# Performance work log

Hardware: AMD Instinct MI355X
Metric: run time of the kernel (lower is better)

The kernel has to match this reference:

```python
import jax, jax.numpy as jnp
import numpy as np

N_NODES = 50000
HIDDEN = 128
IN_DIM = 128
N_EDGES = 1600000


def gcn_conv(x, W, b, src, dst, deg_isqrt, n_nodes):
    # x: [N, Fin], W: [Fin, Fout]. src/dst include self-loops.
    h = x @ W  # [N, Fout]
    norm = deg_isqrt[src] * deg_isqrt[dst]  # [E+N]
    msgs = h[src] * norm[:, None]  # [E+N, Fout]
    agg = jax.ops.segment_sum(msgs, dst, num_segments=n_nodes)
    return agg + b


def setup_inputs() -> dict:
    key = jax.random.key(0)
    ks = jax.random.split(key, 8)
    x = jax.random.normal(ks[0], (N_NODES, IN_DIM), dtype=jnp.float32)
    edge_index = jax.random.randint(ks[1], (2, N_EDGES), 0, N_NODES, dtype=jnp.int64 if jax.config.jax_enable_x64 else jnp.int32)
    s1 = 1.0 / np.sqrt(IN_DIM)
    s2 = 1.0 / np.sqrt(HIDDEN)
    W1 = jax.random.uniform(ks[2], (IN_DIM, HIDDEN), jnp.float32, -s1, s1)
    b1 = jnp.zeros((HIDDEN,), jnp.float32)
    W2 = jax.random.uniform(ks[3], (HIDDEN, HIDDEN), jnp.float32, -s2, s2)
    b2 = jnp.zeros((HIDDEN,), jnp.float32)
    Wc = jax.random.uniform(ks[4], (HIDDEN, 1), jnp.float32, -s2, s2)
    bc = jnp.zeros((1,), jnp.float32)
    return {"x": x, "edge_index": edge_index, "W1": W1, "b1": b1,
            "W2": W2, "b2": b2, "Wc": Wc, "bc": bc}


def reference(x, edge_index, W1, b1, W2, b2, Wc, bc):
    n = x.shape[0]
    # add self-loops (PyG GCNConv default)
    loop = jnp.arange(n, dtype=edge_index.dtype)
    src = jnp.concatenate([edge_index[0], loop])
    dst = jnp.concatenate([edge_index[1], loop])
    # symmetric normalization: deg over augmented dst, edge weight 1
    deg = jax.ops.segment_sum(jnp.ones_like(dst, dtype=x.dtype), dst, num_segments=n)
    deg_isqrt = jnp.where(deg > 0, jax.lax.rsqrt(deg), 0.0)
    h = jax.nn.relu(gcn_conv(x, W1, b1, src, dst, deg_isqrt, n))
    h = jax.nn.relu(gcn_conv(h, W2, b2, src, dst, deg_isqrt, n))
    return (h @ Wc + bc).squeeze(-1)  # [N]
```

## Files before the change

### kernel.cpp

```cpp
#include <hip/hip_runtime.h>
#include <hip/hip_fp16.h>
#include <cstdint>


#define EPBH 4096
#define DCAP 9216

__global__ __launch_bounds__(256) void bucket_hist(const int* __restrict__ dst,
                                                   int* __restrict__ hist,
                                                   int ne, int nb, int nbuck) {
  __shared__ int lh[256];
  lh[threadIdx.x] = 0;
  __syncthreads();
  int base = blockIdx.x * EPBH;
#pragma unroll
  for (int j = 0; j < 16; ++j) {
    int e = base + j * 256 + threadIdx.x;
    if (e < ne) {
      int d = __builtin_nontemporal_load(&dst[e]);
      atomicAdd(&lh[d >> 8], 1);
    }
  }
  __syncthreads();
  if (threadIdx.x < nbuck)
    hist[(size_t)threadIdx.x * nb + blockIdx.x] = lh[threadIdx.x];
}

__global__ void scan_block(const int* __restrict__ in, int* __restrict__ part,
                           int* __restrict__ bsum, int n) {
  __shared__ int s[1024];
  int i = blockIdx.x * 1024 + threadIdx.x;
  int v = (i < n) ? in[i] : 0;
  s[threadIdx.x] = v;
  __syncthreads();
  for (int off = 1; off < 1024; off <<= 1) {
    int t = (threadIdx.x >= (unsigned)off) ? s[threadIdx.x - off] : 0;
    __syncthreads();
    s[threadIdx.x] += t;
    __syncthreads();
  }
  if (i < n) part[i] = s[threadIdx.x] - v;
  if (threadIdx.x == 1023) bsum[blockIdx.x] = s[1023];
}

__global__ void scan_partials(int* __restrict__ bsum, int nb) {
  __shared__ int s[256];
  int v = (threadIdx.x < (unsigned)nb) ? bsum[threadIdx.x] : 0;
  s[threadIdx.x] = v;
  __syncthreads();
  for (int off = 1; off < 256; off <<= 1) {
    int t = (threadIdx.x >= (unsigned)off) ? s[threadIdx.x - off] : 0;
    __syncthreads();
    s[threadIdx.x] += t;
    __syncthreads();
  }
  if (threadIdx.x < (unsigned)nb) bsum[threadIdx.x] = s[threadIdx.x] - v;
}

__global__ void finalize_scan(const int* __restrict__ part, const int* __restrict__ bsum,
                              int* __restrict__ out, int n) {
  int i = blockIdx.x * blockDim.x + threadIdx.x;
  if (i < n) out[i] = part[i] + bsum[i >> 10];
}

__global__ __launch_bounds__(256) void bucket_scatter(const int* __restrict__ src,
                                                      const int* __restrict__ dst,
                                                      const int* __restrict__ scanned,
                                                      uint2* __restrict__ ebuf,
                                                      int ne, int nb, int nbuck) {
  __shared__ int cur[256];
  if (threadIdx.x < nbuck)
    cur[threadIdx.x] = scanned[(size_t)threadIdx.x * nb + blockIdx.x];
  __syncthreads();
  int base = blockIdx.x * EPBH;
#pragma unroll
  for (int j = 0; j < 16; ++j) {
    int e = base + j * 256 + threadIdx.x;
    if (e < ne) {
      int s = __builtin_nontemporal_load(&src[e]);
      int d = __builtin_nontemporal_load(&dst[e]);
      int pos = atomicAdd(&cur[d >> 8], 1);
      ebuf[pos] = make_uint2((unsigned)s, (unsigned)d);
    }
  }
}

__global__ __launch_bounds__(256) void bucket_csr(const uint2* __restrict__ ebuf,
                                                  const int* __restrict__ scanned,
                                                  int* __restrict__ row_ptr,
                                                  float* __restrict__ dinv,
                                                  int* __restrict__ col,
                                                  int ne, int nb, int nbuck, int n) {
  __shared__ int lcnt[256];
  __shared__ int lofs[256];
  __shared__ int cur[256];
  __shared__ uint2 sbuf[DCAP];
  int b = blockIdx.x;
  int start = scanned[(size_t)b * nb];
  int end = (b + 1 < nbuck) ? scanned[(size_t)(b + 1) * nb] : ne;
  lcnt[threadIdx.x] = 0;
  __syncthreads();
  for (int k = start + threadIdx.x; k < end; k += 256) {
    uint2 ed = ebuf[k];
    int rel = k - start;
    if (rel < DCAP) sbuf[rel] = ed;
    atomicAdd(&lcnt[ed.y & 255], 1);
  }
  __syncthreads();
  int v = lcnt[threadIdx.x];
  lofs[threadIdx.x] = v;
  __syncthreads();
  for (int off = 1; off < 256; off <<= 1) {
    int t = (threadIdx.x >= (unsigned)off) ? lofs[threadIdx.x - off] : 0;
    __syncthreads();
    lofs[threadIdx.x] += t;
    __syncthreads();
  }
  int excl = lofs[threadIdx.x] - v;
  int node = b * 256 + threadIdx.x;
  if (node < n) {
    row_ptr[node] = start + excl;
    dinv[node] = rsqrtf((float)(v + 1));
  }
  cur[threadIdx.x] = start + excl;
  __syncthreads();
  for (int k = start + threadIdx.x; k < end; k += 256) {
    int rel = k - start;
    uint2 ed = (rel < DCAP) ? sbuf[rel] : ebuf[k];
    int pos = atomicAdd(&cur[ed.y & 255], 1);
    col[pos] = (int)ed.x;
  }
  if (b == nbuck - 1 && threadIdx.x == 0) row_ptr[n] = ne;
}


typedef _Float16 half_t;
typedef __attribute__((ext_vector_type(8))) _Float16 f16x8;
typedef __attribute__((ext_vector_type(4))) float f32x4;

#define LDP 136

__global__ __launch_bounds__(256) void gemm_mfma_h(const float* __restrict__ in,
                                                   const float* __restrict__ W,
                                                   const float* __restrict__ dinv,
                                                   __half* __restrict__ out, int nrows) {
  __shared__ half_t As[64][LDP];
  __shared__ half_t Bs[128][LDP];
  int tid = threadIdx.x;
  int row0 = blockIdx.x * 64;

#pragma unroll
  for (int it = 0; it < 16; ++it) {
    int idx = it * 256 + tid;
    int k = idx >> 5;
    int f4 = (idx & 31) * 4;
    float4 w = *(const float4*)&W[(size_t)k * 128 + f4];
    Bs[f4 + 0][k] = (half_t)w.x;
    Bs[f4 + 1][k] = (half_t)w.y;
    Bs[f4 + 2][k] = (half_t)w.z;
    Bs[f4 + 3][k] = (half_t)w.w;
  }
#pragma unroll
  for (int it = 0; it < 8; ++it) {
    int idx = it * 256 + tid;
    int r = idx >> 5;
    int k4 = (idx & 31) * 4;
    int grow = row0 + r;
    float4 v = make_float4(0.f, 0.f, 0.f, 0.f);
    if (grow < nrows) v = *(const float4*)&in[(size_t)grow * 128 + k4];
    As[r][k4 + 0] = (half_t)v.x;
    As[r][k4 + 1] = (half_t)v.y;
    As[r][k4 + 2] = (half_t)v.z;
    As[r][k4 + 3] = (half_t)v.w;
  }
  __syncthreads();

  int wv = tid >> 6;
  int lane = tid & 63;
  int m = lane & 15;
  int kg = lane >> 4;

  f32x4 acc[8];
#pragma unroll
  for (int ct = 0; ct < 8; ++ct) acc[ct] = (f32x4){0.f, 0.f, 0.f, 0.f};

#pragma unroll
  for (int ks = 0; ks < 4; ++ks) {
    f16x8 a = *(const f16x8*)&As[wv * 16 + m][ks * 32 + kg * 8];
#pragma unroll
    for (int ct = 0; ct < 8; ++ct) {
      f16x8 b = *(const f16x8*)&Bs[ct * 16 + m][ks * 32 + kg * 8];
      acc[ct] = __builtin_amdgcn_mfma_f32_16x16x32_f16(a, b, acc[ct], 0, 0, 0);
    }
  }

  int orow = row0 + wv * 16 + kg * 4;
  float d0 = (orow + 0 < nrows) ? dinv[orow + 0] : 0.f;
  float d1 = (orow + 1 < nrows) ? dinv[orow + 1] : 0.f;
  float d2 = (orow + 2 < nrows) ? dinv[orow + 2] : 0.f;
  float d3 = (orow + 3 < nrows) ? dinv[orow + 3] : 0.f;
#pragma unroll
  for (int ct = 0; ct < 8; ++ct) {
    int ocol = ct * 16 + m;
    if (orow + 0 < nrows) out[(size_t)(orow + 0) * 128 + ocol] = __float2half_rn(acc[ct][0] * d0);
    if (orow + 1 < nrows) out[(size_t)(orow + 1) * 128 + ocol] = __float2half_rn(acc[ct][1] * d1);
    if (orow + 2 < nrows) out[(size_t)(orow + 2) * 128 + ocol] = __float2half_rn(acc[ct][2] * d2);
    if (orow + 3 < nrows) out[(size_t)(orow + 3) * 128 + ocol] = __float2half_rn(acc[ct][3] * d3);
  }
}


__device__ inline float4 h4_to_f4(uint2 u) {
  __half2 a = *(__half2*)&u.x;
  __half2 b = *(__half2*)&u.y;
  float2 fa = __half22float2(a);
  float2 fb = __half22float2(b);
  return make_float4(fa.x, fa.y, fb.x, fb.y);
}


__global__ __launch_bounds__(256) void aggregate_h(const __half* __restrict__ hsh,
                                                   const int* __restrict__ row_ptr,
                                                   const int* __restrict__ col,
                                                   const float* __restrict__ dinv,
                                                   const float* __restrict__ bias,
                                                   float* __restrict__ out, int n) {
  int node = (blockIdx.x * blockDim.x + threadIdx.x) >> 6;
  if (node >= n) return;
  int lane = threadIdx.x & 63;
  int half_ = lane >> 5;
  int f4 = lane & 31;
  const uint2* rows = (const uint2*)hsh;

  int start = row_ptr[node];
  int end = row_ptr[node + 1];

  float4 acc = make_float4(0.f, 0.f, 0.f, 0.f);
  if (half_ == 0) acc = h4_to_f4(rows[(size_t)node * 32 + f4]);

  int e = start + half_;
  for (; e + 14 < end; e += 16) {
    uint2 u[8];
#pragma unroll
    for (int j = 0; j < 8; ++j) u[j] = rows[(size_t)col[e + 2 * j] * 32 + f4];
#pragma unroll
    for (int j = 0; j < 8; ++j) {
      float4 v = h4_to_f4(u[j]);
      acc.x += v.x; acc.y += v.y; acc.z += v.z; acc.w += v.w;
    }
  }
  for (; e < end; e += 2) {
    float4 v = h4_to_f4(rows[(size_t)col[e] * 32 + f4]);
    acc.x += v.x; acc.y += v.y; acc.z += v.z; acc.w += v.w;
  }

  acc.x += __shfl_xor(acc.x, 32);
  acc.y += __shfl_xor(acc.y, 32);
  acc.z += __shfl_xor(acc.z, 32);
  acc.w += __shfl_xor(acc.w, 32);

  if (half_ == 0) {
    float d = dinv[node];
    float4 b = ((const float4*)bias)[f4];
    float4 o;
    o.x = fmaxf(acc.x * d + b.x, 0.f);
    o.y = fmaxf(acc.y * d + b.y, 0.f);
    o.z = fmaxf(acc.z * d + b.z, 0.f);
    o.w = fmaxf(acc.w * d + b.w, 0.f);
    ((float4*)out)[(size_t)node * 32 + f4] = o;
  }
}


__global__ __launch_bounds__(256) void aggregate_dot_h(const __half* __restrict__ hsh,
                                                       const int* __restrict__ row_ptr,
                                                       const int* __restrict__ col,
                                                       const float* __restrict__ dinv,
                                                       const float* __restrict__ bias,
                                                       const float* __restrict__ Wc,
                                                       const float* __restrict__ bc,
                                                       float* __restrict__ out, int n) {
  int node = (blockIdx.x * blockDim.x + threadIdx.x) >> 6;
  if (node >= n) return;
  int lane = threadIdx.x & 63;
  int half_ = lane >> 5;
  int f4 = lane & 31;
  const uint2* rows = (const uint2*)hsh;

  int start = row_ptr[node];
  int end = row_ptr[node + 1];

  float4 acc = make_float4(0.f, 0.f, 0.f, 0.f);
  if (half_ == 0) acc = h4_to_f4(rows[(size_t)node * 32 + f4]);

  int e = start + half_;
  for (; e + 14 < end; e += 16) {
    uint2 u[8];
#pragma unroll
    for (int j = 0; j < 8; ++j) u[j] = rows[(size_t)col[e + 2 * j] * 32 + f4];
#pragma unroll
    for (int j = 0; j < 8; ++j) {
      float4 v = h4_to_f4(u[j]);
      acc.x += v.x; acc.y += v.y; acc.z += v.z; acc.w += v.w;
    }
  }
  for (; e < end; e += 2) {
    float4 v = h4_to_f4(rows[(size_t)col[e] * 32 + f4]);
    acc.x += v.x; acc.y += v.y; acc.z += v.z; acc.w += v.w;
  }

  acc.x += __shfl_xor(acc.x, 32);
  acc.y += __shfl_xor(acc.y, 32);
  acc.z += __shfl_xor(acc.z, 32);
  acc.w += __shfl_xor(acc.w, 32);

  float d = dinv[node];
  float4 b = ((const float4*)bias)[f4];
  float4 w = ((const float4*)Wc)[f4];
  float s = fmaxf(acc.x * d + b.x, 0.f) * w.x
          + fmaxf(acc.y * d + b.y, 0.f) * w.y
          + fmaxf(acc.z * d + b.z, 0.f) * w.z
          + fmaxf(acc.w * d + b.w, 0.f) * w.w;
#pragma unroll
  for (int off = 16; off; off >>= 1) s += __shfl_xor(s, off);
  if (lane == 0) out[node] = s + bc[0];
}


extern "C" void kernel_launch(void* const* d_in, const int* in_sizes, int n_in,
                              void* d_out, int out_size, void* d_ws, size_t ws_size,
                              hipStream_t stream) {
  const float* x  = (const float*)d_in[0];
  const int* ei   = (const int*)d_in[1];
  const float* W1 = (const float*)d_in[2];
  const float* b1 = (const float*)d_in[3];
  const float* W2 = (const float*)d_in[4];
  const float* b2 = (const float*)d_in[5];
  const float* Wc = (const float*)d_in[6];
  const float* bc = (const float*)d_in[7];
  float* out = (float*)d_out;

  int n  = in_sizes[0] / 128;
  int ne = in_sizes[1] / 2;
  const int* src = ei;
  const int* dst = ei + ne;

  int NBb = (ne + EPBH - 1) / EPBH;
  int NBUCK = (n + 255) >> 8;
  int HN = NBUCK * NBb;

  char* p = (char*)d_ws;
  auto alloc = [&](size_t bytes) {
    char* r = p;
    p += (bytes + 255) & ~(size_t)255;
    return r;
  };
  int*    hist    = (int*)alloc((size_t)HN * 4);
  int*    part    = (int*)alloc((size_t)HN * 4);
  int*    bsum    = (int*)alloc(256 * 4);
  int*    row_ptr = (int*)alloc((size_t)(n + 1) * 4);
  float*  dinv    = (float*)alloc((size_t)n * 4);
  int*    col     = (int*)alloc((size_t)ne * 4);
  __half* hsh     = (__half*)alloc((size_t)n * 128 * 2);
  float*  h1      = (float*)alloc((size_t)n * 128 * 4);
  uint2*  ebuf    = (uint2*)h1;

  bucket_hist<<<NBb, 256, 0, stream>>>(dst, hist, ne, NBb, NBUCK);
  int nsb = (HN + 1023) / 1024;
  scan_block<<<nsb, 1024, 0, stream>>>(hist, part, bsum, HN);
  scan_partials<<<1, 256, 0, stream>>>(bsum, nsb);
  finalize_scan<<<(HN + 255) / 256, 256, 0, stream>>>(part, bsum, hist, HN);
  bucket_scatter<<<NBb, 256, 0, stream>>>(src, dst, hist, ebuf, ne, NBb, NBUCK);
  bucket_csr<<<NBUCK, 256, 0, stream>>>(ebuf, hist, row_ptr, dinv, col, ne, NBb, NBUCK, n);

  int gemm_blocks = (n + 63) / 64;
  int agg_blocks = (n + 3) / 4;

  gemm_mfma_h<<<gemm_blocks, 256, 0, stream>>>(x, W1, dinv, hsh, n);
  aggregate_h<<<agg_blocks, 256, 0, stream>>>(hsh, row_ptr, col, dinv, b1, h1, n);
  gemm_mfma_h<<<gemm_blocks, 256, 0, stream>>>(h1, W2, dinv, hsh, n);
  aggregate_dot_h<<<agg_blocks, 256, 0, stream>>>(hsh, row_ptr, col, dinv, b2, Wc, bc, out, n);
}
```

Measured before the change: 226.4 us.

## Pack edge buffer, drop finalize_scan, store layer-1 output in fp16

Several traffic reductions at once. Each histogram block now handles twice as many edges, which halves the histogram size and the scan work. The finalize_scan kernel is removed; scatter and CSR add the block partials inline. Edges are packed into one 32-bit word (src<<8 | dst&255) in place of a uint2, which halves ebuf traffic and LDS use. The hidden layer between the two convolutions is written as fp16, and a new GEMM variant reads it directly, cutting that tensor's read and write bytes in half. The packing assumes src fits in 24 bits, and fp16 storage of the hidden activations adds rounding error.

```diff
diff --git a/kernel.cpp b/kernel.cpp
--- a/kernel.cpp
+++ b/kernel.cpp
@@ -3,7 +3,7 @@
 #include <cstdint>
 
 
-#define EPBH 4096
+#define EPBH 8192
 #define DCAP 9216
 
 __global__ __launch_bounds__(256) void bucket_hist(const int* __restrict__ dst,
@@ -14,7 +14,7 @@
   __syncthreads();
   int base = blockIdx.x * EPBH;
 #pragma unroll
-  for (int j = 0; j < 16; ++j) {
+  for (int j = 0; j < 32; ++j) {
     int e = base + j * 256 + threadIdx.x;
     if (e < ne) {
       int d = __builtin_nontemporal_load(&dst[e]);
@@ -57,36 +57,35 @@
   if (threadIdx.x < (unsigned)nb) bsum[threadIdx.x] = s[threadIdx.x] - v;
 }
 
-__global__ void finalize_scan(const int* __restrict__ part, const int* __restrict__ bsum,
-                              int* __restrict__ out, int n) {
-  int i = blockIdx.x * blockDim.x + threadIdx.x;
-  if (i < n) out[i] = part[i] + bsum[i >> 10];
-}
 
 __global__ __launch_bounds__(256) void bucket_scatter(const int* __restrict__ src,
                                                       const int* __restrict__ dst,
-                                                      const int* __restrict__ scanned,
-                                                      uint2* __restrict__ ebuf,
+                                                      const int* __restrict__ part,
+                                                      const int* __restrict__ bsum,
+                                                      uint32_t* __restrict__ ebuf,
                                                       int ne, int nb, int nbuck) {
   __shared__ int cur[256];
-  if (threadIdx.x < nbuck)
-    cur[threadIdx.x] = scanned[(size_t)threadIdx.x * nb + blockIdx.x];
+  if (threadIdx.x < nbuck) {
+    int idx = threadIdx.x * nb + blockIdx.x;
+    cur[threadIdx.x] = part[idx] + bsum[idx >> 10];
+  }
   __syncthreads();
   int base = blockIdx.x * EPBH;
 #pragma unroll
-  for (int j = 0; j < 16; ++j) {
+  for (int j = 0; j < 32; ++j) {
     int e = base + j * 256 + threadIdx.x;
     if (e < ne) {
       int s = __builtin_nontemporal_load(&src[e]);
       int d = __builtin_nontemporal_load(&dst[e]);
       int pos = atomicAdd(&cur[d >> 8], 1);
-      ebuf[pos] = make_uint2((unsigned)s, (unsigned)d);
+      ebuf[pos] = ((uint32_t)s << 8) | (uint32_t)(d & 255);
     }
   }
 }
 
-__global__ __launch_bounds__(256) void bucket_csr(const uint2* __restrict__ ebuf,
-                                                  const int* __restrict__ scanned,
+__global__ __launch_bounds__(256) void bucket_csr(const uint32_t* __restrict__ ebuf,
+                                                  const int* __restrict__ part,
+                                                  const int* __restrict__ bsum,
                                                   int* __restrict__ row_ptr,
                                                   float* __restrict__ dinv,
                                                   int* __restrict__ col,
@@ -94,17 +93,22 @@
   __shared__ int lcnt[256];
   __shared__ int lofs[256];
   __shared__ int cur[256];
-  __shared__ uint2 sbuf[DCAP];
+  __shared__ uint32_t sbuf[DCAP];
   int b = blockIdx.x;
-  int start = scanned[(size_t)b * nb];
-  int end = (b + 1 < nbuck) ? scanned[(size_t)(b + 1) * nb] : ne;
+  int i0 = b * nb;
+  int start = part[i0] + bsum[i0 >> 10];
+  int end = ne;
+  if (b + 1 < nbuck) {
+    int i1 = (b + 1) * nb;
+    end = part[i1] + bsum[i1 >> 10];
+  }
   lcnt[threadIdx.x] = 0;
   __syncthreads();
   for (int k = start + threadIdx.x; k < end; k += 256) {
-    uint2 ed = ebuf[k];
+    uint32_t ed = ebuf[k];
     int rel = k - start;
     if (rel < DCAP) sbuf[rel] = ed;
-    atomicAdd(&lcnt[ed.y & 255], 1);
+    atomicAdd(&lcnt[ed & 255u], 1);
   }
   __syncthreads();
   int v = lcnt[threadIdx.x];
@@ -126,9 +130,9 @@
   __syncthreads();
   for (int k = start + threadIdx.x; k < end; k += 256) {
     int rel = k - start;
-    uint2 ed = (rel < DCAP) ? sbuf[rel] : ebuf[k];
-    int pos = atomicAdd(&cur[ed.y & 255], 1);
-    col[pos] = (int)ed.x;
+    uint32_t ed = (rel < DCAP) ? sbuf[rel] : ebuf[k];
+    int pos = atomicAdd(&cur[ed & 255u], 1);
+    col[pos] = (int)(ed >> 8);
   }
   if (b == nbuck - 1 && threadIdx.x == 0) row_ptr[n] = ne;
 }
@@ -140,15 +144,45 @@
 
 #define LDP 136
 
-__global__ __launch_bounds__(256) void gemm_mfma_h(const float* __restrict__ in,
-                                                   const float* __restrict__ W,
-                                                   const float* __restrict__ dinv,
-                                                   __half* __restrict__ out, int nrows) {
-  __shared__ half_t As[64][LDP];
-  __shared__ half_t Bs[128][LDP];
-  int tid = threadIdx.x;
-  int row0 = blockIdx.x * 64;
-
+__device__ __forceinline__ void gemm_core(half_t (*As)[LDP], half_t (*Bs)[LDP],
+                                          const float* __restrict__ dinv,
+                                          __half* __restrict__ out,
+                                          int row0, int nrows, int tid) {
+  int wv = tid >> 6;
+  int lane = tid & 63;
+  int m = lane & 15;
+  int kg = lane >> 4;
+
+  f32x4 acc[8];
+#pragma unroll
+  for (int ct = 0; ct < 8; ++ct) acc[ct] = (f32x4){0.f, 0.f, 0.f, 0.f};
+
+#pragma unroll
+  for (int ks = 0; ks < 4; ++ks) {
+    f16x8 a = *(const f16x8*)&As[wv * 16 + m][ks * 32 + kg * 8];
+#pragma unroll
+    for (int ct = 0; ct < 8; ++ct) {
+      f16x8 b = *(const f16x8*)&Bs[ct * 16 + m][ks * 32 + kg * 8];
+      acc[ct] = __builtin_amdgcn_mfma_f32_16x16x32_f16(a, b, acc[ct], 0, 0, 0);
+    }
+  }
+
+  int orow = row0 + wv * 16 + kg * 4;
+  float d0 = (orow + 0 < nrows) ? dinv[orow + 0] : 0.f;
+  float d1 = (orow + 1 < nrows) ? dinv[orow + 1] : 0.f;
+  float d2 = (orow + 2 < nrows) ? dinv[orow + 2] : 0.f;
+  float d3 = (orow + 3 < nrows) ? dinv[orow + 3] : 0.f;
+#pragma unroll
+  for (int ct = 0; ct < 8; ++ct) {
+    int ocol = ct * 16 + m;
+    if (orow + 0 < nrows) out[(size_t)(orow + 0) * 128 + ocol] = __float2half_rn(acc[ct][0] * d0);
+    if (orow + 1 < nrows) out[(size_t)(orow + 1) * 128 + ocol] = __float2half_rn(acc[ct][1] * d1);
+    if (orow + 2 < nrows) out[(size_t)(orow + 2) * 128 + ocol] = __float2half_rn(acc[ct][2] * d2);
+    if (orow + 3 < nrows) out[(size_t)(orow + 3) * 128 + ocol] = __float2half_rn(acc[ct][3] * d3);
+  }
+}
+
+__device__ __forceinline__ void stage_W(half_t (*Bs)[LDP], const float* __restrict__ W, int tid) {
 #pragma unroll
   for (int it = 0; it < 16; ++it) {
     int idx = it * 256 + tid;
@@ -160,6 +194,17 @@
     Bs[f4 + 2][k] = (half_t)w.z;
     Bs[f4 + 3][k] = (half_t)w.w;
   }
+}
+
+__global__ __launch_bounds__(256) void gemm_mfma_f32in(const float* __restrict__ in,
+                                                       const float* __restrict__ W,
+                                                       const float* __restrict__ dinv,
+                                                       __half* __restrict__ out, int nrows) {
+  __shared__ half_t As[64][LDP];
+  __shared__ half_t Bs[128][LDP];
+  int tid = threadIdx.x;
+  int row0 = blockIdx.x * 64;
+  stage_W(Bs, W, tid);
 #pragma unroll
   for (int it = 0; it < 8; ++it) {
     int idx = it * 256 + tid;
@@ -174,39 +219,30 @@
     As[r][k4 + 3] = (half_t)v.w;
   }
   __syncthreads();
-
-  int wv = tid >> 6;
-  int lane = tid & 63;
-  int m = lane & 15;
-  int kg = lane >> 4;
-
-  f32x4 acc[8];
-#pragma unroll
-  for (int ct = 0; ct < 8; ++ct) acc[ct] = (f32x4){0.f, 0.f, 0.f, 0.f};
-
-#pragma unroll
-  for (int ks = 0; ks < 4; ++ks) {
-    f16x8 a = *(const f16x8*)&As[wv * 16 + m][ks * 32 + kg * 8];
-#pragma unroll
-    for (int ct = 0; ct < 8; ++ct) {
-      f16x8 b = *(const f16x8*)&Bs[ct * 16 + m][ks * 32 + kg * 8];
-      acc[ct] = __builtin_amdgcn_mfma_f32_16x16x32_f16(a, b, acc[ct], 0, 0, 0);
-    }
-  }
-
-  int orow = row0 + wv * 16 + kg * 4;
-  float d0 = (orow + 0 < nrows) ? dinv[orow + 0] : 0.f;
-  float d1 = (orow + 1 < nrows) ? dinv[orow + 1] : 0.f;
-  float d2 = (orow + 2 < nrows) ? dinv[orow + 2] : 0.f;
-  float d3 = (orow + 3 < nrows) ? dinv[orow + 3] : 0.f;
-#pragma unroll
-  for (int ct = 0; ct < 8; ++ct) {
-    int ocol = ct * 16 + m;
-    if (orow + 0 < nrows) out[(size_t)(orow + 0) * 128 + ocol] = __float2half_rn(acc[ct][0] * d0);
-    if (orow + 1 < nrows) out[(size_t)(orow + 1) * 128 + ocol] = __float2half_rn(acc[ct][1] * d1);
-    if (orow + 2 < nrows) out[(size_t)(orow + 2) * 128 + ocol] = __float2half_rn(acc[ct][2] * d2);
-    if (orow + 3 < nrows) out[(size_t)(orow + 3) * 128 + ocol] = __float2half_rn(acc[ct][3] * d3);
-  }
+  gemm_core(As, Bs, dinv, out, row0, nrows, tid);
+}
+
+__global__ __launch_bounds__(256) void gemm_mfma_f16in(const __half* __restrict__ in,
+                                                       const float* __restrict__ W,
+                                                       const float* __restrict__ dinv,
+                                                       __half* __restrict__ out, int nrows) {
+  __shared__ half_t As[64][LDP];
+  __shared__ half_t Bs[128][LDP];
+  int tid = threadIdx.x;
+  int row0 = blockIdx.x * 64;
+  stage_W(Bs, W, tid);
+#pragma unroll
+  for (int it = 0; it < 4; ++it) {
+    int idx = it * 256 + tid;
+    int r = idx >> 4;
+    int k8 = (idx & 15) * 8;
+    int grow = row0 + r;
+    uint4 v = make_uint4(0u, 0u, 0u, 0u);
+    if (grow < nrows) v = *(const uint4*)&in[(size_t)grow * 128 + k8];
+    *(uint4*)&As[r][k8] = v;
+  }
+  __syncthreads();
+  gemm_core(As, Bs, dinv, out, row0, nrows, tid);
 }
 
 
@@ -224,7 +260,7 @@
                                                    const int* __restrict__ col,
                                                    const float* __restrict__ dinv,
                                                    const float* __restrict__ bias,
-                                                   float* __restrict__ out, int n) {
+                                                   __half* __restrict__ out, int n) {
   int node = (blockIdx.x * blockDim.x + threadIdx.x) >> 6;
   if (node >= n) return;
   int lane = threadIdx.x & 63;
@@ -262,12 +298,10 @@
   if (half_ == 0) {
     float d = dinv[node];
     float4 b = ((const float4*)bias)[f4];
-    float4 o;
-    o.x = fmaxf(acc.x * d + b.x, 0.f);
-    o.y = fmaxf(acc.y * d + b.y, 0.f);
-    o.z = fmaxf(acc.z * d + b.z, 0.f);
-    o.w = fmaxf(acc.w * d + b.w, 0.f);
-    ((float4*)out)[(size_t)node * 32 + f4] = o;
+    __half2 h01 = __floats2half2_rn(fmaxf(acc.x * d + b.x, 0.f), fmaxf(acc.y * d + b.y, 0.f));
+    __half2 h23 = __floats2half2_rn(fmaxf(acc.z * d + b.z, 0.f), fmaxf(acc.w * d + b.w, 0.f));
+    uint2 o = make_uint2(*(uint*)&h01, *(uint*)&h23);
+    ((uint2*)out)[(size_t)node * 32 + f4] = o;
   }
 }
 
@@ -362,22 +396,21 @@
   float*  dinv    = (float*)alloc((size_t)n * 4);
   int*    col     = (int*)alloc((size_t)ne * 4);
   __half* hsh     = (__half*)alloc((size_t)n * 128 * 2);
-  float*  h1      = (float*)alloc((size_t)n * 128 * 4);
-  uint2*  ebuf    = (uint2*)h1;
+  __half* h1      = (__half*)alloc((size_t)n * 128 * 2);
+  uint32_t* ebuf  = (uint32_t*)alloc((size_t)ne * 4);
 
   bucket_hist<<<NBb, 256, 0, stream>>>(dst, hist, ne, NBb, NBUCK);
   int nsb = (HN + 1023) / 1024;
   scan_block<<<nsb, 1024, 0, stream>>>(hist, part, bsum, HN);
   scan_partials<<<1, 256, 0, stream>>>(bsum, nsb);
-  finalize_scan<<<(HN + 255) / 256, 256, 0, stream>>>(part, bsum, hist, HN);
-  bucket_scatter<<<NBb, 256, 0, stream>>>(src, dst, hist, ebuf, ne, NBb, NBUCK);
-  bucket_csr<<<NBUCK, 256, 0, stream>>>(ebuf, hist, row_ptr, dinv, col, ne, NBb, NBUCK, n);
+  bucket_scatter<<<NBb, 256, 0, stream>>>(src, dst, part, bsum, ebuf, ne, NBb, NBUCK);
+  bucket_csr<<<NBUCK, 256, 0, stream>>>(ebuf, part, bsum, row_ptr, dinv, col, ne, NBb, NBUCK, n);
 
   int gemm_blocks = (n + 63) / 64;
   int agg_blocks = (n + 3) / 4;
 
-  gemm_mfma_h<<<gemm_blocks, 256, 0, stream>>>(x, W1, dinv, hsh, n);
+  gemm_mfma_f32in<<<gemm_blocks, 256, 0, stream>>>(x, W1, dinv, hsh, n);
   aggregate_h<<<agg_blocks, 256, 0, stream>>>(hsh, row_ptr, col, dinv, b1, h1, n);
-  gemm_mfma_h<<<gemm_blocks, 256, 0, stream>>>(h1, W2, dinv, hsh, n);
+  gemm_mfma_f16in<<<gemm_blocks, 256, 0, stream>>>(h1, W2, dinv, hsh, n);
   aggregate_dot_h<<<agg_blocks, 256, 0, stream>>>(hsh, row_ptr, col, dinv, b2, Wc, bc, out, n);
 }
```

Measured after the change: 229.3 us. Within noise of the previous version (+1.3%).
